# Performance work log

Hardware: AMD Instinct MI355X
Metric: run time of the kernel (lower is better)

## Reference

```python
import jax, jax.numpy as jnp
import numpy as np

N, E, DIM = 50000, 500000, 64
EIN3, EIN4 = 16, 16

def setup_inputs() -> dict:
    key = jax.random.key(0)
    ks = jax.random.split(key, 8)
    x = jax.random.normal(ks[0], (N, DIM), dtype=jnp.float32)
    edge_index3 = jax.random.randint(ks[1], (2, E), 0, N, dtype=jnp.int64)
    edge_attr3 = jax.random.normal(ks[2], (E, EIN3), dtype=jnp.float32)
    edge_attr4 = jax.random.normal(ks[3], (E, EIN4), dtype=jnp.float32)
    batch = jnp.zeros((N,), dtype=jnp.int64)
    # MLP params: Linear(2*dim, 4*dim) -> ReLU -> Linear(4*dim, 1)
    W1 = jax.random.normal(ks[4], (2 * DIM, 4 * DIM), dtype=jnp.float32) / np.sqrt(2 * DIM)
    b1 = jnp.zeros((4 * DIM,), dtype=jnp.float32)
    W2 = jax.random.normal(ks[5], (4 * DIM, 1), dtype=jnp.float32) / np.sqrt(4 * DIM)
    b2 = jnp.zeros((1,), dtype=jnp.float32)
    return {"x": x, "edge_index3": edge_index3, "edge_attr3": edge_attr3,
            "edge_attr4": edge_attr4, "batch": batch,
            "W1": W1, "b1": b1, "W2": W2, "b2": b2}

def reference(x, edge_index3, edge_attr3, edge_attr4, batch, W1, b1, W2, b2):
    # gather endpoints: temp[k] = x[edge_index3[k]] -> [E, dim]
    src = x[edge_index3[0]]  # [E, dim]
    dst = x[edge_index3[1]]  # [E, dim]
    # symmetric concat: [[src|dst], [dst|src]] -> [2E, 2*dim]
    yhat = jnp.concatenate([
        jnp.concatenate([src, dst], axis=1),
        jnp.concatenate([dst, src], axis=1)], axis=0)
    h = jax.nn.relu(yhat @ W1 + b1)        # [2E, 4*dim]
    y = (h @ W2 + b2)[:, 0]                # [2E]
    return y.reshape(2, -1).mean(axis=0)   # [E]
```

## Files before the change

### kernel.cpp

```cpp
#include <hip/hip_runtime.h>

#define DIM 64
#define HID 256
#define ROWB 512
#define QSCALE  25.4f
#define DQSCALE (5.0f/127.0f)

typedef short s8v __attribute__((ext_vector_type(8)));
typedef float f4v __attribute__((ext_vector_type(4)));

union U16 { uint4 u; s8v s; };

__device__ __forceinline__ unsigned short bf16_rne(float f) {
    unsigned u = __float_as_uint(f);
    u = (u + 0x7fffu + ((u >> 16) & 1u)) >> 16;
    return (unsigned short)u;
}
__device__ __forceinline__ unsigned pk_bf16(float a, float b) {
    return (unsigned)bf16_rne(a) | ((unsigned)bf16_rne(b) << 16);
}

#define DPP_ADD(x, ctrl, rmask)                                               \
    (x) += __int_as_float(__builtin_amdgcn_update_dpp(                        \
        0, __float_as_int(x), (ctrl), (rmask), 0xf, true))
__device__ __forceinline__ float wave_sum64(float x) {
    DPP_ADD(x, 0x111, 0xf);
    DPP_ADD(x, 0x112, 0xf);
    DPP_ADD(x, 0x114, 0xf);
    DPP_ADD(x, 0x118, 0xf);
    DPP_ADD(x, 0x142, 0xa);
    DPP_ADD(x, 0x143, 0xc);
    return x;
}

__global__ __launch_bounds__(256) void prep_wfrag(
    const float* __restrict__ W1, unsigned short* __restrict__ wf)
{
    const int f = blockIdx.x * 256 + threadIdx.x;
    if (f >= 32 * 2 * 64) return;
    const int lane = f & 63;
    const int t    = (f >> 6) & 1;
    const int ct   = f >> 7;
    const int col  = ct * 16 + (lane & 15);
    const int k0   = t * 32 + (lane >> 4) * 8;
    const float* __restrict__ wsrc =
        W1 + ((col >= HID) ? (DIM * HID + col - HID) : col);
    unsigned short v[8];
#pragma unroll
    for (int j = 0; j < 8; ++j) v[j] = bf16_rne(wsrc[(size_t)(k0 + j) * HID]);
    uint4 o;
    o.x = (unsigned)v[0] | ((unsigned)v[1] << 16);
    o.y = (unsigned)v[2] | ((unsigned)v[3] << 16);
    o.z = (unsigned)v[4] | ((unsigned)v[5] << 16);
    o.w = (unsigned)v[6] | ((unsigned)v[7] << 16);
    *(uint4*)(wf + (size_t)f * 8) = o;
}

__global__ __launch_bounds__(256) void node_mfma_q(
    const float* __restrict__ x, const unsigned short* __restrict__ wf,
    const float* __restrict__ b1, unsigned char* __restrict__ tab, int n)
{
    const int lane    = threadIdx.x & 63;
    const int w       = threadIdx.x >> 6;
    const int rowgrp  = w >> 1;
    const int colhalf = w & 1;
    const int m       = lane & 15;
    const int quad    = lane >> 4;
    const int rbase   = blockIdx.x * 32 + rowgrp * 16;

    const int arow = rbase + m;
    const float* __restrict__ xr = x + (size_t)((arow < n) ? arow : (n - 1)) * DIM;
    s8v a[2];
#pragma unroll
    for (int t = 0; t < 2; ++t) {
        const float4 lo = *(const float4*)(xr + t * 32 + quad * 8);
        const float4 hi = *(const float4*)(xr + t * 32 + quad * 8 + 4);
        U16 u;
        u.u.x = pk_bf16(lo.x, lo.y);
        u.u.y = pk_bf16(lo.z, lo.w);
        u.u.z = pk_bf16(hi.x, hi.y);
        u.u.w = pk_bf16(hi.z, hi.w);
        a[t] = u.s;
    }

    const uint4* __restrict__ wfv = (const uint4*)wf;

    f4v acc[16];
#pragma unroll
    for (int ct = 0; ct < 16; ++ct) {
        const int ctg = colhalf * 16 + ct;
        U16 b0u, b1u;
        b0u.u = wfv[(ctg * 2 + 0) * 64 + lane];
        b1u.u = wfv[(ctg * 2 + 1) * 64 + lane];
        f4v c = {0.f, 0.f, 0.f, 0.f};
        c = __builtin_amdgcn_mfma_f32_16x16x32_bf16(a[0], b0u.s, c, 0, 0, 0);
        c = __builtin_amdgcn_mfma_f32_16x16x32_bf16(a[1], b1u.s, c, 0, 0, 0);
        if (colhalf == 0) {
            const float bias = b1[ctg * 16 + m];
            c[0] += bias; c[1] += bias; c[2] += bias; c[3] += bias;
        }
        acc[ct] = c;
    }

#pragma unroll
    for (int r = 0; r < 4; ++r) {
        const int gr = rbase + quad * 4 + r;
        if (gr >= n) continue;
        unsigned b[16];
#pragma unroll
        for (int ct = 0; ct < 16; ++ct) {
            float v = __builtin_rintf(acc[ct][r] * QSCALE);
            v = fminf(fmaxf(v, -127.f), 127.f);
            b[ct] = (unsigned)((int)v) & 255u;
        }
        uint4 o;
        o.x = b[0]  | (b[1]  << 8) | (b[2]  << 16) | (b[3]  << 24);
        o.y = b[4]  | (b[5]  << 8) | (b[6]  << 16) | (b[7]  << 24);
        o.z = b[8]  | (b[9]  << 8) | (b[10] << 16) | (b[11] << 24);
        o.w = b[12] | (b[13] << 8) | (b[14] << 16) | (b[15] << 24);
        *(uint4*)(tab + (size_t)gr * ROWB + colhalf * 256 + m * 16) = o;
    }
}

__global__ __launch_bounds__(256) void edge_mlp_q(
    const int* __restrict__ ei, const unsigned char* __restrict__ tab,
    const float* __restrict__ W2, const float* __restrict__ b2,
    float* __restrict__ out, int ne)
{
    const int lane = threadIdx.x & 63;
    const int lx   = lane ^ 32;
    const int wid  = blockIdx.x * (blockDim.x >> 6) + (threadIdx.x >> 6);
    const int nw   = gridDim.x * (blockDim.x >> 6);
    const int lp   = lane & 31;
    const int mcol = lp >> 1;
    const int ctb  = (lp & 1) * 8;
    float wv[8];
#pragma unroll
    for (int k = 0; k < 8; ++k) wv[k] = W2[(ctb + k) * 16 + mcol];
    const float bias = b2[0];

    for (int e0 = wid * 4; e0 < ne; e0 += nw * 4) {
        const int eu = __builtin_amdgcn_readfirstlane(e0);
        uint2 hs[4], hd[4];
#pragma unroll
        for (int q = 0; q < 4; ++q) {
            const int s = ei[eu + q];
            const int d = ei[ne + eu + q];
            hs[q] = *(const uint2*)(tab + (size_t)s * ROWB + 8 * lane);
            hd[q] = *(const uint2*)(tab + (size_t)d * ROWB + 8 * lx);
        }
        float p[4];
#pragma unroll
        for (int q = 0; q < 4; ++q) {
            float acc = 0.f;
#pragma unroll
            for (int k = 0; k < 4; ++k) {
                const int as = (int)(signed char)(hs[q].x >> (8 * k));
                const int bd = (int)(signed char)(hd[q].x >> (8 * k));
                const int t  = max(as + bd, 0);
                acc = fmaf((float)t, wv[k], acc);
            }
#pragma unroll
            for (int k = 0; k < 4; ++k) {
                const int as = (int)(signed char)(hs[q].y >> (8 * k));
                const int bd = (int)(signed char)(hd[q].y >> (8 * k));
                const int t  = max(as + bd, 0);
                acc = fmaf((float)t, wv[4 + k], acc);
            }
            p[q] = wave_sum64(acc);
        }
        if (lane == 63) {
            const float sc = 0.5f * DQSCALE;
            *(float4*)(out + e0) = make_float4(
                sc * p[0] + bias, sc * p[1] + bias,
                sc * p[2] + bias, sc * p[3] + bias);
        }
    }
}

extern "C" void kernel_launch(void* const* d_in, const int* in_sizes, int n_in,
                              void* d_out, int out_size, void* d_ws, size_t ws_size,
                              hipStream_t stream) {
    const float* x  = (const float*)d_in[0];
    const int*   ei = (const int*)d_in[1];
    const float* W1 = (const float*)d_in[5];
    const float* b1 = (const float*)d_in[6];
    const float* W2 = (const float*)d_in[7];
    const float* b2 = (const float*)d_in[8];
    float* out = (float*)d_out;

    const int n  = in_sizes[0] / DIM;
    const int ne = in_sizes[1] / 2;

    unsigned char*  tab = (unsigned char*)d_ws;
    unsigned short* wf  = (unsigned short*)(tab + (size_t)n * ROWB);

    prep_wfrag<<<16, 256, 0, stream>>>(W1, wf);
    node_mfma_q<<<(n + 31) / 32, 256, 0, stream>>>(x, wf, b1, tab, n);
    edge_mlp_q<<<8192, 256, 0, stream>>>(ei, tab, W2, b2, out, ne);
}
```

Measured before the change: 186.4 us.

## Store biased uint8 node table and split edge kernel into two launches

Node table entries are stored as unsigned bytes offset by 128, so the edge kernel can convert bytes to float directly and apply ReLU as fmax against 256 in float. A constant correction term (256 times the sum of W2, scaled) is subtracted once per output, removing the sign-extension and int-to-float work per element. The edge pass is also split into two launches over halves of the edges with half the grid each, which adds launch overhead and may hurt or help cache locality.

```diff
diff --git a/kernel.cpp b/kernel.cpp
--- a/kernel.cpp
+++ b/kernel.cpp
@@ -32,6 +32,8 @@
     DPP_ADD(x, 0x143, 0xc);
     return x;
 }
+
+#define UB2F(u, k) ((float)(((u) >> (8 * (k))) & 0xffu))
 
 __global__ __launch_bounds__(256) void prep_wfrag(
     const float* __restrict__ W1, unsigned short* __restrict__ wf)
@@ -111,7 +113,7 @@
         for (int ct = 0; ct < 16; ++ct) {
             float v = __builtin_rintf(acc[ct][r] * QSCALE);
             v = fminf(fmaxf(v, -127.f), 127.f);
-            b[ct] = (unsigned)((int)v) & 255u;
+            b[ct] = (unsigned)((int)v + 128) & 255u;
         }
         uint4 o;
         o.x = b[0]  | (b[1]  << 8) | (b[2]  << 16) | (b[3]  << 24);
@@ -125,7 +127,7 @@
 __global__ __launch_bounds__(256) void edge_mlp_q(
     const int* __restrict__ ei, const unsigned char* __restrict__ tab,
     const float* __restrict__ W2, const float* __restrict__ b2,
-    float* __restrict__ out, int ne)
+    float* __restrict__ out, int ne, int e0v, int e1v)
 {
     const int lane = threadIdx.x & 63;
     const int lx   = lane ^ 32;
@@ -137,9 +139,11 @@
     float wv[8];
 #pragma unroll
     for (int k = 0; k < 8; ++k) wv[k] = W2[(ctb + k) * 16 + mcol];
+    float wsum = wv[0] + wv[1] + wv[2] + wv[3] + wv[4] + wv[5] + wv[6] + wv[7];
+    wsum = wave_sum64(wsum);
     const float bias = b2[0];
 
-    for (int e0 = wid * 4; e0 < ne; e0 += nw * 4) {
+    for (int e0 = e0v + wid * 4; e0 < e1v; e0 += nw * 4) {
         const int eu = __builtin_amdgcn_readfirstlane(e0);
         uint2 hs[4], hd[4];
 #pragma unroll
@@ -155,25 +159,22 @@
             float acc = 0.f;
 #pragma unroll
             for (int k = 0; k < 4; ++k) {
-                const int as = (int)(signed char)(hs[q].x >> (8 * k));
-                const int bd = (int)(signed char)(hd[q].x >> (8 * k));
-                const int t  = max(as + bd, 0);
-                acc = fmaf((float)t, wv[k], acc);
+                const float t = fmaxf(UB2F(hs[q].x, k) + UB2F(hd[q].x, k), 256.0f);
+                acc = fmaf(t, wv[k], acc);
             }
 #pragma unroll
             for (int k = 0; k < 4; ++k) {
-                const int as = (int)(signed char)(hs[q].y >> (8 * k));
-                const int bd = (int)(signed char)(hd[q].y >> (8 * k));
-                const int t  = max(as + bd, 0);
-                acc = fmaf((float)t, wv[4 + k], acc);
+                const float t = fmaxf(UB2F(hs[q].y, k) + UB2F(hd[q].y, k), 256.0f);
+                acc = fmaf(t, wv[4 + k], acc);
             }
             p[q] = wave_sum64(acc);
         }
         if (lane == 63) {
             const float sc = 0.5f * DQSCALE;
+            const float corr = bias - sc * 256.0f * wsum;
             *(float4*)(out + e0) = make_float4(
-                sc * p[0] + bias, sc * p[1] + bias,
-                sc * p[2] + bias, sc * p[3] + bias);
+                sc * p[0] + corr, sc * p[1] + corr,
+                sc * p[2] + corr, sc * p[3] + corr);
         }
     }
 }
@@ -197,5 +198,7 @@
 
     prep_wfrag<<<16, 256, 0, stream>>>(W1, wf);
     node_mfma_q<<<(n + 31) / 32, 256, 0, stream>>>(x, wf, b1, tab, n);
-    edge_mlp_q<<<8192, 256, 0, stream>>>(ei, tab, W2, b2, out, ne);
-}
+    const int half = (ne / 2) & ~3;
+    edge_mlp_q<<<4096, 256, 0, stream>>>(ei, tab, W2, b2, out, ne, 0, half);
+    edge_mlp_q<<<4096, 256, 0, stream>>>(ei, tab, W2, b2, out, ne, half, ne);
+}
```

New measurement: 192.6 us. +3.4%, slower.
